# Performance work log

Hardware: AMD Instinct MI355X
Metric: run time of the kernel (lower is better)

The kernel has to match this reference:

```python
import jax, jax.numpy as jnp
import numpy as np

NUM_BINS = 15
THRESHOLD = 0.01


def setup_inputs() -> dict:
    key = jax.random.key(0)
    k1, k2 = jax.random.split(key)
    N, C = 500000, 100
    probas = jax.random.uniform(k1, (N, C), dtype=jnp.float32)
    labels = jax.random.randint(k2, (N,), 0, C, dtype=jnp.int64)
    return {"probas": probas, "labels": labels}


def reference(probas, labels):
    # probas: [N, C] float, labels: [N] int
    N, C = probas.shape
    B = NUM_BINS
    bins = jnp.linspace(0.0, 1.0, B + 1, dtype=probas.dtype)  # [B+1]

    # bin index: bins[lo] <= p < bins[lo+1] (side='right' => right edge strict)
    lo = jnp.searchsorted(bins, probas, side='right') - 1      # [N, C]
    lo_c = jnp.clip(lo, 0, B - 1)
    left_edge = bins[lo_c]
    # original uses strict inequalities on BOTH edges, plus threshold filter
    valid = (probas > THRESHOLD) & (lo >= 0) & (lo < B) & (probas > left_edge)
    w = valid.astype(probas.dtype)                              # [N, C]

    # segment id = class * B + bin, flattened over [N, C]
    cols = jnp.broadcast_to(jnp.arange(C), (N, C))
    seg = (cols * B + lo_c).ravel()
    num_seg = C * B

    correct = (labels[:, None] == jnp.arange(C)[None, :]).astype(probas.dtype)

    count = jax.ops.segment_sum(w.ravel(), seg, num_segments=num_seg)
    sum_p = jax.ops.segment_sum((probas * w).ravel(), seg, num_segments=num_seg)
    sum_a = jax.ops.segment_sum((correct * w).ravel(), seg, num_segments=num_seg)

    nan = jnp.asarray(jnp.nan, probas.dtype)
    denom = jnp.maximum(count, 1.0)
    confs = jnp.where(count > 0, sum_p / denom, nan).reshape(C, B)
    accs = jnp.where(count > 0, sum_a / denom, nan).reshape(C, B)
    n_samples = count.reshape(C, B)
    return confs, accs, n_samples
```

## Files before the change

kernel.cpp:

```cpp
#include <hip/hip_runtime.h>

#define NBINS 15
#define NCLS  100
#define NSEG  (NBINS * NCLS)
#define NGRP  64
#define MAXBLK 2048
#define BLK   256
#define SUMSCALE 2048.0f
#define INV15 (1.0f / 15.0f)

__global__ __launch_bounds__(BLK) void calib_accum(
    const float* __restrict__ probas,
    const int*   __restrict__ labels,
    float*       __restrict__ partA,
    int total4)
{
    __shared__ unsigned int s_pk[NSEG];
    __shared__ unsigned int s_ac[NSEG];
    const int t = threadIdx.x;
    for (int i = t; i < NSEG; i += BLK) { s_pk[i] = 0u; s_ac[i] = 0u; }
    __syncthreads();

    const float4* __restrict__ p4 = (const float4*)probas;
    const int stride = gridDim.x * BLK;

    for (int i = blockIdx.x * BLK + t; i < total4; i += stride) {
        float4 v = p4[i];
        int row  = i / 25;
        int col0 = (i - row * 25) * 4;
        int lbl  = labels[row];
        float pv[4] = {v.x, v.y, v.z, v.w};
        #pragma unroll
        for (int j = 0; j < 4; ++j) {
            float p = pv[j];
            int c = col0 + j;
            int k = (int)(p * 15.0f);
            if (k < NBINS && (float)(k + 1) * INV15 <= p)      ++k;
            else if (k > 0 && (float)k * INV15 > p)            --k;
            float left = (float)k * INV15;
            if (p > 0.01f && k < NBINS && p > left) {
                int seg = c * NBINS + k;
                unsigned int pk = (1u << 20) | (unsigned int)(p * SUMSCALE + 0.5f);
                atomicAdd(&s_pk[seg], pk);
                if (lbl == c) atomicAdd(&s_ac[seg], 1u);
            }
        }
    }
    __syncthreads();

    float* dst = partA + (size_t)blockIdx.x * (3 * NSEG);
    for (int s = t; s < NSEG; s += BLK) {
        unsigned int pk = s_pk[s];
        dst[s]            = (float)(pk >> 20);
        dst[NSEG + s]     = (float)(pk & 0xFFFFFu) * (1.0f / SUMSCALE);
        dst[2 * NSEG + s] = (float)s_ac[s];
    }
}

__global__ __launch_bounds__(256) void calib_mid(
    const float* __restrict__ partA, int nblk, int chunk,
    float*       __restrict__ partB)
{
    int t = blockIdx.x * 256 + threadIdx.x;
    if (t >= NGRP * NSEG) return;
    int g = t / NSEG;
    int s = t - g * NSEG;
    int b0 = g * chunk;
    int b1 = b0 + chunk; if (b1 > nblk) b1 = nblk;
    float cnt = 0.f, sum = 0.f, acc = 0.f;
    for (int b = b0; b < b1; ++b) {
        const float* src = partA + (size_t)b * (3 * NSEG);
        cnt += src[s];
        sum += src[NSEG + s];
        acc += src[2 * NSEG + s];
    }
    float* dst = partB + (size_t)g * (3 * NSEG);
    dst[s]            = cnt;
    dst[NSEG + s]     = sum;
    dst[2 * NSEG + s] = acc;
}

__global__ __launch_bounds__(256) void calib_fin(
    const float* __restrict__ partB,
    float*       __restrict__ out)
{
    int s = blockIdx.x * 256 + threadIdx.x;
    if (s >= NSEG) return;
    float cnt = 0.f, sum = 0.f, acc = 0.f;
    #pragma unroll
    for (int g = 0; g < NGRP; ++g) {
        const float* src = partB + g * (3 * NSEG);
        cnt += src[s];
        sum += src[NSEG + s];
        acc += src[2 * NSEG + s];
    }
    float conf, accv;
    if (cnt > 0.f) { conf = sum / cnt; accv = acc / cnt; }
    else { conf = __int_as_float(0x7fc00000); accv = conf; }
    out[s]            = conf;
    out[NSEG + s]     = accv;
    out[2 * NSEG + s] = cnt;
}

extern "C" void kernel_launch(void* const* d_in, const int* in_sizes, int n_in,
                              void* d_out, int out_size, void* d_ws, size_t ws_size,
                              hipStream_t stream) {
    const float* probas = (const float*)d_in[0];
    const int*   labels = (const int*)d_in[1];
    float* out = (float*)d_out;
    float* ws  = (float*)d_ws;

    int total  = in_sizes[0];
    int total4 = total / 4;

    size_t ws_floats = ws_size / sizeof(float);
    long long avail = (long long)ws_floats - (long long)NGRP * 3 * NSEG;
    int nblk = (int)(avail / (3 * NSEG));
    if (nblk > MAXBLK) nblk = MAXBLK;
    if (nblk < 1) nblk = 1;

    float* partA = ws;
    float* partB = ws + (size_t)nblk * (3 * NSEG);

    calib_accum<<<nblk, BLK, 0, stream>>>(probas, labels, partA, total4);
    int chunk = (nblk + NGRP - 1) / NGRP;
    calib_mid<<<(NGRP * NSEG + 255) / 256, 256, 0, stream>>>(partA, nblk, chunk, partB);
    calib_fin<<<(NSEG + 255) / 256, 256, 0, stream>>>(partB, out);
}
```

Measured before the change: 293.5 us.

## Use nontemporal dual-stream loads and keep packed integer partials through the reduction

After: 285.1 us. -2.9%, faster.

```diff
diff --git a/kernel.cpp b/kernel.cpp
--- a/kernel.cpp
+++ b/kernel.cpp
@@ -9,10 +9,37 @@
 #define SUMSCALE 2048.0f
 #define INV15 (1.0f / 15.0f)
 
+typedef float nf4 __attribute__((ext_vector_type(4)));
+
+__device__ __forceinline__ void proc_f4(nf4 v, int i,
+                                        const int* __restrict__ labels,
+                                        unsigned int* s_pk, unsigned int* s_ac)
+{
+    int row  = i / 25;
+    int col0 = (i - row * 25) * 4;
+    int lbl  = labels[row];
+    float pv[4] = {v.x, v.y, v.z, v.w};
+    #pragma unroll
+    for (int j = 0; j < 4; ++j) {
+        float p = pv[j];
+        int c = col0 + j;
+        int k = (int)(p * 15.0f);
+        if (k < NBINS && (float)(k + 1) * INV15 <= p)      ++k;
+        else if (k > 0 && (float)k * INV15 > p)            --k;
+        float left = (float)k * INV15;
+        if (p > 0.01f && k < NBINS && p > left) {
+            int seg = c * NBINS + k;
+            unsigned int pk = (1u << 20) | (unsigned int)(p * SUMSCALE + 0.5f);
+            atomicAdd(&s_pk[seg], pk);
+            if (lbl == c) atomicAdd(&s_ac[seg], 1u);
+        }
+    }
+}
+
 __global__ __launch_bounds__(BLK) void calib_accum(
     const float* __restrict__ probas,
     const int*   __restrict__ labels,
-    float*       __restrict__ partA,
+    unsigned int* __restrict__ partU,
     int total4)
 {
     __shared__ unsigned int s_pk[NSEG];
@@ -21,45 +48,31 @@
     for (int i = t; i < NSEG; i += BLK) { s_pk[i] = 0u; s_ac[i] = 0u; }
     __syncthreads();
 
-    const float4* __restrict__ p4 = (const float4*)probas;
+    const nf4* __restrict__ p4 = (const nf4*)probas;
     const int stride = gridDim.x * BLK;
+    const int half4  = total4 >> 1;
 
-    for (int i = blockIdx.x * BLK + t; i < total4; i += stride) {
-        float4 v = p4[i];
-        int row  = i / 25;
-        int col0 = (i - row * 25) * 4;
-        int lbl  = labels[row];
-        float pv[4] = {v.x, v.y, v.z, v.w};
-        #pragma unroll
-        for (int j = 0; j < 4; ++j) {
-            float p = pv[j];
-            int c = col0 + j;
-            int k = (int)(p * 15.0f);
-            if (k < NBINS && (float)(k + 1) * INV15 <= p)      ++k;
-            else if (k > 0 && (float)k * INV15 > p)            --k;
-            float left = (float)k * INV15;
-            if (p > 0.01f && k < NBINS && p > left) {
-                int seg = c * NBINS + k;
-                unsigned int pk = (1u << 20) | (unsigned int)(p * SUMSCALE + 0.5f);
-                atomicAdd(&s_pk[seg], pk);
-                if (lbl == c) atomicAdd(&s_ac[seg], 1u);
-            }
-        }
+    for (int i = blockIdx.x * BLK + t; i < half4; i += stride) {
+        nf4 a = __builtin_nontemporal_load(&p4[i]);
+        nf4 b = __builtin_nontemporal_load(&p4[i + half4]);
+        proc_f4(a, i,         labels, s_pk, s_ac);
+        proc_f4(b, i + half4, labels, s_pk, s_ac);
+    }
+    if ((total4 & 1) && blockIdx.x == 0 && t == 0) {
+        proc_f4(p4[total4 - 1], total4 - 1, labels, s_pk, s_ac);
     }
     __syncthreads();
 
-    float* dst = partA + (size_t)blockIdx.x * (3 * NSEG);
+    unsigned int* dst = partU + (size_t)blockIdx.x * (2 * NSEG);
     for (int s = t; s < NSEG; s += BLK) {
-        unsigned int pk = s_pk[s];
-        dst[s]            = (float)(pk >> 20);
-        dst[NSEG + s]     = (float)(pk & 0xFFFFFu) * (1.0f / SUMSCALE);
-        dst[2 * NSEG + s] = (float)s_ac[s];
+        dst[s]        = s_pk[s];
+        dst[NSEG + s] = s_ac[s];
     }
 }
 
 __global__ __launch_bounds__(256) void calib_mid(
-    const float* __restrict__ partA, int nblk, int chunk,
-    float*       __restrict__ partB)
+    const unsigned int* __restrict__ partU, int nblk, int chunk,
+    unsigned int*       __restrict__ partB)
 {
     int t = blockIdx.x * 256 + threadIdx.x;
     if (t >= NGRP * NSEG) return;
@@ -67,39 +80,46 @@
     int s = t - g * NSEG;
     int b0 = g * chunk;
     int b1 = b0 + chunk; if (b1 > nblk) b1 = nblk;
-    float cnt = 0.f, sum = 0.f, acc = 0.f;
+    unsigned int cnt = 0u, sumq = 0u, acc = 0u;
     for (int b = b0; b < b1; ++b) {
-        const float* src = partA + (size_t)b * (3 * NSEG);
-        cnt += src[s];
-        sum += src[NSEG + s];
-        acc += src[2 * NSEG + s];
+        const unsigned int* src = partU + (size_t)b * (2 * NSEG);
+        unsigned int pk = src[s];
+        cnt  += pk >> 20;
+        sumq += pk & 0xFFFFFu;
+        acc  += src[NSEG + s];
     }
-    float* dst = partB + (size_t)g * (3 * NSEG);
+    unsigned int* dst = partB + (size_t)g * (3 * NSEG);
     dst[s]            = cnt;
-    dst[NSEG + s]     = sum;
+    dst[NSEG + s]     = sumq;
     dst[2 * NSEG + s] = acc;
 }
 
 __global__ __launch_bounds__(256) void calib_fin(
-    const float* __restrict__ partB,
-    float*       __restrict__ out)
+    const unsigned int* __restrict__ partB,
+    float*              __restrict__ out)
 {
     int s = blockIdx.x * 256 + threadIdx.x;
     if (s >= NSEG) return;
-    float cnt = 0.f, sum = 0.f, acc = 0.f;
+    unsigned int cnt = 0u, sumq = 0u, acc = 0u;
     #pragma unroll
     for (int g = 0; g < NGRP; ++g) {
-        const float* src = partB + g * (3 * NSEG);
-        cnt += src[s];
-        sum += src[NSEG + s];
-        acc += src[2 * NSEG + s];
+        const unsigned int* src = partB + g * (3 * NSEG);
+        cnt  += src[s];
+        sumq += src[NSEG + s];
+        acc  += src[2 * NSEG + s];
     }
     float conf, accv;
-    if (cnt > 0.f) { conf = sum / cnt; accv = acc / cnt; }
-    else { conf = __int_as_float(0x7fc00000); accv = conf; }
+    if (cnt > 0u) {
+        float inv = 1.0f / (float)cnt;
+        conf = (float)sumq * (1.0f / SUMSCALE) * inv;
+        accv = (float)acc * inv;
+    } else {
+        conf = __int_as_float(0x7fc00000);
+        accv = conf;
+    }
     out[s]            = conf;
     out[NSEG + s]     = accv;
-    out[2 * NSEG + s] = cnt;
+    out[2 * NSEG + s] = (float)cnt;
 }
 
 extern "C" void kernel_launch(void* const* d_in, const int* in_sizes, int n_in,
@@ -108,22 +128,22 @@
     const float* probas = (const float*)d_in[0];
     const int*   labels = (const int*)d_in[1];
     float* out = (float*)d_out;
-    float* ws  = (float*)d_ws;
+    unsigned int* ws = (unsigned int*)d_ws;
 
     int total  = in_sizes[0];
     int total4 = total / 4;
 
-    size_t ws_floats = ws_size / sizeof(float);
-    long long avail = (long long)ws_floats - (long long)NGRP * 3 * NSEG;
-    int nblk = (int)(avail / (3 * NSEG));
+    size_t ws_u32 = ws_size / sizeof(unsigned int);
+    long long avail = (long long)ws_u32 - (long long)NGRP * 3 * NSEG;
+    int nblk = (int)(avail / (2 * NSEG));
     if (nblk > MAXBLK) nblk = MAXBLK;
     if (nblk < 1) nblk = 1;
 
-    float* partA = ws;
-    float* partB = ws + (size_t)nblk * (3 * NSEG);
+    unsigned int* partU = ws;
+    unsigned int* partB = ws + (size_t)nblk * (2 * NSEG);
 
-    calib_accum<<<nblk, BLK, 0, stream>>>(probas, labels, partA, total4);
+    calib_accum<<<nblk, BLK, 0, stream>>>(probas, labels, partU, total4);
     int chunk = (nblk + NGRP - 1) / NGRP;
-    calib_mid<<<(NGRP * NSEG + 255) / 256, 256, 0, stream>>>(partA, nblk, chunk, partB);
+    calib_mid<<<(NGRP * NSEG + 255) / 256, 256, 0, stream>>>(partU, nblk, chunk, partB);
     calib_fin<<<(NSEG + 255) / 256, 256, 0, stream>>>(partB, out);
 }
```
